# Kernel optimization log

Measured on AMD Instinct MI355X. Metric: run time of the kernel, lower is better.

The kernel has to match this reference:

```python
import jax, jax.numpy as jnp
import numpy as np

B, H, S, D = 4, 16, 2048, 64


def setup_inputs() -> dict:
    key = jax.random.key(0)
    kq, kk, kv = jax.random.split(key, 3)
    q = jax.random.normal(kq, (B, H, S, D), dtype=jnp.float32)
    k = jax.random.normal(kk, (B, H, S, D), dtype=jnp.float32)
    v = jax.random.normal(kv, (B, H, S, D), dtype=jnp.float32)
    return {"q": q, "k": k, "v": v, "num_k": 170}


def reference(q, k, v, num_k):
    d_tensor = k.shape[-1]
    # [B,H,S,S] score matrix
    score = jnp.einsum("bhqd,bhkd->bhqk", q, k) / jnp.sqrt(jnp.float32(d_tensor))
    nk = min(int(num_k), k.shape[2])
    if nk:
        # kth-largest value per query row acts as threshold
        top_vals = jax.lax.top_k(score, nk)[0]          # [B,H,S,nk]
        thresh = top_vals[..., -1:]                      # [B,H,S,1]
        score = jnp.where(score < thresh, jnp.float32(-1e18), score)
    attn = jax.nn.softmax(score, axis=-1)
    return jnp.einsum("bhqk,bhkd->bhqd", attn, v)
```

## Files before the change

### kernel.cpp

```cpp
#include <hip/hip_runtime.h>
#include <math.h>

#define S_LEN 2048
#define DHEAD 64
#define NBINS 512
#define BPL (NBINS / 64)
#define CANDMAX 48
#define NBH 64
#define NROWS (NBH * S_LEN)
#define VT_BYTES (64ull * DHEAD * S_LEN * 2)

typedef _Float16 f16x8 __attribute__((ext_vector_type(8)));
typedef _Float16 f16x4 __attribute__((ext_vector_type(4)));
typedef float    f32x4 __attribute__((ext_vector_type(4)));

__global__ __launch_bounds__(256)
void prep_vt(const float* __restrict__ V, _Float16* __restrict__ VT) {
  const int bh  = (int)blockIdx.x >> 3;
  const int dg8 = (int)blockIdx.x & 7;
  const int t   = (int)threadIdx.x;
  const int dim = dg8 * 8 + (t >> 5);
  const int kc  = t & 31;
  const float* Vb = V + (size_t)bh * (S_LEN * DHEAD);
  _Float16* VTb = VT + ((size_t)bh * DHEAD + dim) * S_LEN;
  for (int i = 0; i < 8; ++i) {
    int key0 = (kc + i * 32) * 8;
    f16x8 h;
    #pragma unroll
    for (int j = 0; j < 8; ++j)
      h[j] = (_Float16)Vb[(size_t)(key0 + j) * DHEAD + dim];
    *(f16x8*)(VTb + key0) = h;
  }
}

__global__ __launch_bounds__(256, 4)
void qk_kernel(const float* __restrict__ Q, const float* __restrict__ K,
               float* __restrict__ Sws, int row0) {
  __shared__ __align__(16) char kbuf[32768];
  f16x8* Khw = (f16x8*)kbuf;
  f16x8* Klw = (f16x8*)(kbuf + 16384);

  const int tid  = (int)threadIdx.x;
  const int lane = tid & 63;
  const int wid  = tid >> 6;
  const int nxl  = (int)gridDim.x >> 3;
  const int xcd  = (int)blockIdx.x & 7;
  const int lb   = (int)blockIdx.x >> 3;
  const int rb   = lb >> 1;
  const int kb   = lb & 1;
  const int rowl = xcd * (nxl * 32) + rb * 64 + wid * 16;
  const int rowg = row0 + rowl;
  const int bh   = rowg >> 11;
  const int key0 = kb * 1024;

  const int g = lane >> 4;
  const int m = lane & 15;

  f16x8 a_hi0, a_lo0, a_hi1, a_lo1;
  {
    const float* Qrow = Q + (size_t)(rowg + m) * DHEAD;
    float4 qa = *(const float4*)(Qrow + g * 8);
    float4 qb = *(const float4*)(Qrow + g * 8 + 4);
    float4 qc = *(const float4*)(Qrow + 32 + g * 8);
    float4 qd = *(const float4*)(Qrow + 32 + g * 8 + 4);
    float x[16] = {qa.x,qa.y,qa.z,qa.w, qb.x,qb.y,qb.z,qb.w,
                   qc.x,qc.y,qc.z,qc.w, qd.x,qd.y,qd.z,qd.w};
    #pragma unroll
    for (int j = 0; j < 8; ++j) {
      _Float16 h0 = (_Float16)x[j];
      a_hi0[j] = h0;  a_lo0[j] = (_Float16)(x[j] - (float)h0);
      _Float16 h1 = (_Float16)x[8 + j];
      a_hi1[j] = h1;  a_lo1[j] = (_Float16)(x[8 + j] - (float)h1);
    }
  }

  const float* Kb = K + (size_t)bh * (S_LEN * DHEAD);
  float* Srow = Sws + (size_t)rowl * S_LEN;

  const int skey  = tid >> 1;
  const int shalf = tid & 1;
  const int ssw   = skey & 7;

  float4 pf[8];
  {
    const float4* kr = (const float4*)(Kb + (size_t)(key0 + skey) * DHEAD + shalf * 32);
    #pragma unroll
    for (int j = 0; j < 8; ++j) pf[j] = kr[j];
  }

  for (int t = 0; t < 8; ++t) {
    #pragma unroll
    for (int jj = 0; jj < 4; ++jj) {
      float x[8] = {pf[2*jj].x, pf[2*jj].y, pf[2*jj].z, pf[2*jj].w,
                    pf[2*jj+1].x, pf[2*jj+1].y, pf[2*jj+1].z, pf[2*jj+1].w};
      f16x8 hi, lo;
      #pragma unroll
      for (int j = 0; j < 8; ++j) {
        _Float16 h = (_Float16)x[j];
        hi[j] = h;
        lo[j] = (_Float16)(x[j] - (float)h);
      }
      int c = shalf * 4 + jj;
      Khw[skey * 8 + (c ^ ssw)] = hi;
      Klw[skey * 8 + (c ^ ssw)] = lo;
    }
    if (t + 1 < 8) {
      const float4* kr = (const float4*)(Kb + (size_t)(key0 + (t + 1) * 128 + skey) * DHEAD + shalf * 32);
      #pragma unroll
      for (int j = 0; j < 8; ++j) pf[j] = kr[j];
    }
    __syncthreads();

    const f16x8* Kh = (const f16x8*)kbuf;
    const f16x8* Kl = (const f16x8*)(kbuf + 16384);
    int slot0 = ( g      ^ (m & 7));
    int slot1 = ((4 + g) ^ (m & 7));
    #pragma unroll
    for (int p = 0; p < 8; ++p) {
      int keyr = p * 16 + m;
      f16x8 b_hi0 = Kh[keyr * 8 + slot0];
      f16x8 b_hi1 = Kh[keyr * 8 + slot1];
      f16x8 b_lo0 = Kl[keyr * 8 + slot0];
      f16x8 b_lo1 = Kl[keyr * 8 + slot1];
      f32x4 acc = {0.f, 0.f, 0.f, 0.f};
      acc = __builtin_amdgcn_mfma_f32_16x16x32_f16(a_hi0, b_hi0, acc, 0, 0, 0);
      acc = __builtin_amdgcn_mfma_f32_16x16x32_f16(a_hi1, b_hi1, acc, 0, 0, 0);
      acc = __builtin_amdgcn_mfma_f32_16x16x32_f16(a_hi0, b_lo0, acc, 0, 0, 0);
      acc = __builtin_amdgcn_mfma_f32_16x16x32_f16(a_hi1, b_lo1, acc, 0, 0, 0);
      acc = __builtin_amdgcn_mfma_f32_16x16x32_f16(a_lo0, b_hi0, acc, 0, 0, 0);
      acc = __builtin_amdgcn_mfma_f32_16x16x32_f16(a_lo1, b_hi1, acc, 0, 0, 0);
      acc = __builtin_amdgcn_mfma_f32_16x16x32_f16(a_lo0, b_lo0, acc, 0, 0, 0);
      acc = __builtin_amdgcn_mfma_f32_16x16x32_f16(a_lo1, b_lo1, acc, 0, 0, 0);
      int col = key0 + t * 128 + p * 16 + m;
      #pragma unroll
      for (int rg = 0; rg < 4; ++rg)
        __builtin_nontemporal_store(acc[rg] * 0.125f,
            &Srow[(size_t)(g * 4 + rg) * S_LEN + col]);
    }
    __syncthreads();
  }
}

__global__ __launch_bounds__(512, 4)
void selmm_kernel(const float* __restrict__ Sws, const _Float16* __restrict__ VT,
                  const int* __restrict__ nkp, float* __restrict__ Out, int row0) {
  __shared__ unsigned histS[8][NBINS];
  __shared__ float candS[8][CANDMAX];
  __shared__ unsigned candCnt[8];
  __shared__ float psumS[16];
  __shared__ __align__(16) char pbuf[8192];
  __shared__ __align__(16) float4 redS[4][64];

  const int tid  = (int)threadIdx.x;
  const int lane = tid & 63;
  const int wid  = tid >> 6;
  const int nxl  = (int)gridDim.x >> 3;
  const int xcd  = (int)blockIdx.x & 7;
  const int lbk  = (int)blockIdx.x >> 3;
  const int rowlb = xcd * (nxl * 16) + lbk * 16;
  const int rowgb = row0 + rowlb;
  const int bh    = rowgb >> 11;

  int nk = nkp[0];
  if (nk > S_LEN) nk = S_LEN;

  unsigned* hw = histS[wid];
  float sarr[2][32];
  float thr2[2], vmx2[2];

  #pragma unroll
  for (int rr = 0; rr < 2; ++rr) {
    const int rloc = wid * 2 + rr;
    {
      const f32x4* S4 = (const f32x4*)(Sws + (size_t)(rowlb + rloc) * S_LEN);
      #pragma unroll
      for (int j = 0; j < 8; ++j) {
        f32x4 v4 = __builtin_nontemporal_load(S4 + j * 64 + lane);
        sarr[rr][j*4+0] = v4[0]; sarr[rr][j*4+1] = v4[1];
        sarr[rr][j*4+2] = v4[2]; sarr[rr][j*4+3] = v4[3];
      }
    }

    float vmax = -INFINITY, vmin = INFINITY;
    #pragma unroll
    for (int q = 0; q < 32; ++q) {
      vmax = fmaxf(vmax, sarr[rr][q]); vmin = fminf(vmin, sarr[rr][q]);
    }
    #pragma unroll
    for (int off = 32; off >= 1; off >>= 1) {
      vmax = fmaxf(vmax, __shfl_xor(vmax, off));
      vmin = fminf(vmin, __shfl_xor(vmin, off));
    }

    float thresh = -INFINITY;
    if (nk > 0) {
      float range = vmax - vmin;
      float scale = (range > 0.f) ? ((float)NBINS / range) : 0.f;
      float boff  = vmin * scale;

      #pragma unroll
      for (int i2 = 0; i2 < BPL; ++i2) hw[(i2 << 6) | lane] = 0u;
      #pragma unroll
      for (int q = 0; q < 32; ++q) {
        int bb = (int)fmaf(sarr[rr][q], scale, -boff);
        bb = bb < 0 ? 0 : (bb > NBINS - 1 ? NBINS - 1 : bb);
        atomicAdd(&hw[((bb & 7) << 6) | (bb >> 3)], 1u);
      }

      unsigned A = 0;
      #pragma unroll
      for (int i2 = 0; i2 < BPL; ++i2) A += hw[(i2 << 6) | lane];
      unsigned ssum = A;
      #pragma unroll
      for (int off = 1; off <= 32; off <<= 1) {
        unsigned u = (unsigned)__shfl_down((int)ssum, off);
        if (lane + off < 64) ssum += u;
      }
      unsigned cum = ssum - A;
      int bsel = -1; int mloc = 0; int nbloc = 0;
      #pragma unroll
      for (int i2 = BPL - 1; i2 >= 0; --i2) {
        unsigned c0 = cum; cum += hw[(i2 << 6) | lane];
        if (bsel < 0 && c0 < (unsigned)nk && cum >= (unsigned)nk) {
          bsel = (lane << 3) | i2; mloc = nk - (int)c0; nbloc = (int)(cum - c0);
        }
      }
      unsigned long long fm = __ballot(bsel >= 0);
      int srcl = __ffsll(fm) - 1;
      bsel = __shfl(bsel, srcl);
      int mth  = __shfl(mloc, srcl);
      int nbin = __shfl(nbloc, srcl);

      if (nbin <= CANDMAX) {
        if (lane == 0) candCnt[wid] = 0u;
        __builtin_amdgcn_wave_barrier();
        #pragma unroll
        for (int q = 0; q < 32; ++q) {
          int bb = (int)fmaf(sarr[rr][q], scale, -boff);
          bb = bb < 0 ? 0 : (bb > NBINS - 1 ? NBINS - 1 : bb);
          if (bb == bsel) {
            unsigned ix = atomicAdd(&candCnt[wid], 1u);
            if (ix < CANDMAX) candS[wid][ix] = sarr[rr][q];
          }
        }
        __builtin_amdgcn_wave_barrier();
        float prev = INFINITY, kth = -INFINITY;
        int got = 0, guard = 0;
        while (got < mth && guard++ <= CANDMAX) {
          float best = -INFINITY;
          for (int i = 0; i < nbin; ++i) {
            float v = candS[wid][i];
            if (v < prev && v > best) best = v;
          }
          int ce = 0;
          for (int i = 0; i < nbin; ++i) if (candS[wid][i] == best) ce++;
          got += ce; prev = best; kth = best;
        }
        thresh = kth;
      } else {
        unsigned inbin = 0;
        #pragma unroll
        for (int q = 0; q < 32; ++q) {
          int bb = (int)fmaf(sarr[rr][q], scale, -boff);
          bb = bb < 0 ? 0 : (bb > NBINS - 1 ? NBINS - 1 : bb);
          if (bb == bsel) inbin |= (1u << q);
        }
        while (true) {
          float cmax = -INFINITY;
          #pragma unroll
          for (int q = 0; q < 32; ++q) if (inbin & (1u << q)) cmax = fmaxf(cmax, sarr[rr][q]);
          #pragma unroll
          for (int off = 32; off >= 1; off >>= 1) cmax = fmaxf(cmax, __shfl_xor(cmax, off));
          int cnt = 0;
          #pragma unroll
          for (int q = 0; q < 32; ++q) if ((inbin & (1u << q)) && sarr[rr][q] == cmax) cnt++;
          #pragma unroll
          for (int off = 32; off >= 1; off >>= 1) cnt += __shfl_xor(cnt, off);
          if (mth <= cnt) { thresh = cmax; break; }
          mth -= cnt;
          #pragma unroll
          for (int q = 0; q < 32; ++q) if ((inbin & (1u << q)) && sarr[rr][q] == cmax) inbin &= ~(1u << q);
        }
      }
    }
    thr2[rr] = thresh; vmx2[rr] = vmax;

    float psum = 0.f;
    #pragma unroll
    for (int q = 0; q < 32; ++q) {
      float s = sarr[rr][q];
      psum += (s >= thresh) ? __expf(s - vmax) : 0.f;
    }
    #pragma unroll
    for (int off = 32; off >= 1; off >>= 1) psum += __shfl_xor(psum, off);
    if (lane == 0) psumS[rloc] = psum;
  }
  __syncthreads();

  const int g   = lane >> 4;
  const int n16 = lane & 15;
  const int dg  = wid & 3;
  const int kh  = wid >> 2;
  const _Float16* VTb = VT + (size_t)bh * (DHEAD * S_LEN);
  f32x4 acc = {0.f, 0.f, 0.f, 0.f};

  #pragma unroll
  for (int kt = 0; kt < 8; ++kt) {
    #pragma unroll
    for (int rr = 0; rr < 2; ++rr) {
      const int row = wid * 2 + rr;
      f16x4 pv;
      #pragma unroll
      for (int c = 0; c < 4; ++c) {
        float s = sarr[rr][kt * 4 + c];
        float p = (s >= thr2[rr]) ? __expf(s - vmx2[rr]) : 0.f;
        pv[c] = (_Float16)p;
      }
      *(f16x4*)(pbuf + ((row * 512 + lane * 8) ^ ((row & 7) << 4))) = pv;
    }
    __syncthreads();
    #pragma unroll
    for (int s = 0; s < 4; ++s) {
      f16x8 af = *(const f16x8*)(pbuf +
          ((n16 * 512 + kh * 256 + s * 64 + g * 16) ^ ((n16 & 7) << 4)));
      f16x8 bf = *(const f16x8*)(VTb + (size_t)(dg * 16 + n16) * S_LEN +
                                 kt * 256 + kh * 128 + s * 32 + g * 8);
      acc = __builtin_amdgcn_mfma_f32_16x16x32_f16(af, bf, acc, 0, 0, 0);
    }
    __syncthreads();
  }

  if (kh == 1) {
    redS[dg][lane] = make_float4(acc[0], acc[1], acc[2], acc[3]);
  }
  __syncthreads();
  if (kh == 0) {
    float4 o = redS[dg][lane];
    float ov[4] = {o.x, o.y, o.z, o.w};
    #pragma unroll
    for (int rg = 0; rg < 4; ++rg) {
      int row = g * 4 + rg;
      float val = (acc[rg] + ov[rg]) / psumS[row];
      Out[(size_t)(rowgb + row) * DHEAD + dg * 16 + n16] = val;
    }
  }
}

#define TQ 16
#define KT 128
#define NTILES (S_LEN / KT)
#define THREADS 512
#define LCAP 256
#define SOFF   0
#define KHI    131072
#define KLO    147456
#define HOFF   131072
#define KLOFF  147456
#define PLOFF  155648

__global__ __launch_bounds__(THREADS, 2)
void dpsa_kernel(const float* __restrict__ Q, const float* __restrict__ K,
                 const float* __restrict__ V, const int* __restrict__ nkp,
                 float* __restrict__ Out) {
  __shared__ __align__(16) char smem[163840];
  float* Sf = (float*)(smem + SOFF);

  const int tid  = (int)threadIdx.x;
  const int lane = tid & 63;
  const int wid  = tid >> 6;
  const int bid  = (int)blockIdx.x;
  const int bh   = bid >> 7;
  const int qblk = bid & 127;
  const size_t base = (size_t)bh * (size_t)(S_LEN * DHEAD);
  const float* Kbh = K + base;
  const float* Vbh = V + base;

  int nk = nkp[0];
  if (nk > S_LEN) nk = S_LEN;

  const int g = lane >> 4;
  const int m = lane & 15;

  f16x8 a_hi0, a_lo0, a_hi1, a_lo1;
  {
    const float* Qrow = Q + base + (size_t)(qblk * TQ + m) * DHEAD;
    float4 qa = *(const float4*)(Qrow + g * 8);
    float4 qb = *(const float4*)(Qrow + g * 8 + 4);
    float4 qc = *(const float4*)(Qrow + 32 + g * 8);
    float4 qd = *(const float4*)(Qrow + 32 + g * 8 + 4);
    float x[16] = {qa.x,qa.y,qa.z,qa.w, qb.x,qb.y,qb.z,qb.w,
                   qc.x,qc.y,qc.z,qc.w, qd.x,qd.y,qd.z,qd.w};
    #pragma unroll
    for (int j = 0; j < 8; ++j) {
      _Float16 h0 = (_Float16)x[j];
      a_hi0[j] = h0;  a_lo0[j] = (_Float16)(x[j] - (float)h0);
      _Float16 h1 = (_Float16)x[8 + j];
      a_hi1[j] = h1;  a_lo1[j] = (_Float16)(x[8 + j] - (float)h1);
    }
  }

  const f16x8* Kh = (const f16x8*)(smem + KHI);
  const f16x8* Kl = (const f16x8*)(smem + KLO);
  const int keyl = tid >> 2;
  const int q4i  = tid & 3;
  const int sw   = keyl & 7;

  float4 pf0, pf1, pf2, pf3;
  {
    const float4* Kg4 = (const float4*)Kbh;
    int idx = keyl * 16 + q4i * 4;
    pf0 = Kg4[idx]; pf1 = Kg4[idx + 1]; pf2 = Kg4[idx + 2]; pf3 = Kg4[idx + 3];
  }

  for (int t = 0; t < NTILES; ++t) {
    {
      float x[16] = {pf0.x,pf0.y,pf0.z,pf0.w, pf1.x,pf1.y,pf1.z,pf1.w,
                     pf2.x,pf2.y,pf2.z,pf2.w, pf3.x,pf3.y,pf3.z,pf3.w};
      f16x8 hi0, hi1, lo0, lo1;
      #pragma unroll
      for (int j = 0; j < 8; ++j) {
        _Float16 h0 = (_Float16)x[j];
        hi0[j] = h0;  lo0[j] = (_Float16)(x[j] - (float)h0);
        _Float16 h1 = (_Float16)x[8 + j];
        hi1[j] = h1;  lo1[j] = (_Float16)(x[8 + j] - (float)h1);
      }
      f16x8* KhwF = (f16x8*)(smem + KHI);
      f16x8* KlwF = (f16x8*)(smem + KLO);
      KhwF[keyl * 8 + ((q4i * 2)     ^ sw)] = hi0;
      KhwF[keyl * 8 + ((q4i * 2 + 1) ^ sw)] = hi1;
      KlwF[keyl * 8 + ((q4i * 2)     ^ sw)] = lo0;
      KlwF[keyl * 8 + ((q4i * 2 + 1) ^ sw)] = lo1;
    }
    if (t + 1 < NTILES) {
      const float4* Kg4 = (const float4*)(Kbh + (size_t)(t + 1) * (KT * DHEAD));
      int idx = keyl * 16 + q4i * 4;
      pf0 = Kg4[idx]; pf1 = Kg4[idx + 1]; pf2 = Kg4[idx + 2]; pf3 = Kg4[idx + 3];
    }
    __syncthreads();
    {
      int keyr = wid * 16 + m;
      int s0 = ( g      ^ (m & 7));
      int s1 = ((4 + g) ^ (m & 7));
      f16x8 b_hi0 = Kh[keyr * 8 + s0];
      f16x8 b_hi1 = Kh[keyr * 8 + s1];
      f16x8 b_lo0 = Kl[keyr * 8 + s0];
      f16x8 b_lo1 = Kl[keyr * 8 + s1];
      f32x4 acc = {0.f, 0.f, 0.f, 0.f};
      acc = __builtin_amdgcn_mfma_f32_16x16x32_f16(a_hi0, b_hi0, acc, 0, 0, 0);
      acc = __builtin_amdgcn_mfma_f32_16x16x32_f16(a_hi1, b_hi1, acc, 0, 0, 0);
      acc = __builtin_amdgcn_mfma_f32_16x16x32_f16(a_hi0, b_lo0, acc, 0, 0, 0);
      acc = __builtin_amdgcn_mfma_f32_16x16x32_f16(a_hi1, b_lo1, acc, 0, 0, 0);
      acc = __builtin_amdgcn_mfma_f32_16x16x32_f16(a_lo0, b_hi0, acc, 0, 0, 0);
      acc = __builtin_amdgcn_mfma_f32_16x16x32_f16(a_lo1, b_hi1, acc, 0, 0, 0);
      int keyabs = t * KT + wid * 16 + m;
      #pragma unroll
      for (int rg = 0; rg < 4; ++rg)
        Sf[(size_t)(g * 4 + rg) * S_LEN + keyabs] = acc[rg] * 0.125f;
    }
    __syncthreads();
  }

  unsigned* hw = (unsigned*)(smem + HOFF)  + wid * NBINS;
  unsigned* kl = (unsigned*)(smem + KLOFF) + wid * LCAP;
  float*    pl = (float*)(smem + PLOFF)    + wid * LCAP;
  const float4* S4 = (const float4*)(smem + SOFF);

  for (int rr = 0; rr < 2; ++rr) {
    const int row = wid * 2 + rr;
    float sarr[32];
    #pragma unroll
    for (int j = 0; j < 8; ++j) {
      float4 v4 = S4[row * (S_LEN / 4) + j * 64 + lane];
      sarr[j*4+0] = v4.x; sarr[j*4+1] = v4.y;
      sarr[j*4+2] = v4.z; sarr[j*4+3] = v4.w;
    }

    float vmax = -INFINITY, vmin = INFINITY;
    #pragma unroll
    for (int q = 0; q < 32; ++q) {
      vmax = fmaxf(vmax, sarr[q]); vmin = fminf(vmin, sarr[q]);
    }
    #pragma unroll
    for (int off = 32; off >= 1; off >>= 1) {
      vmax = fmaxf(vmax, __shfl_xor(vmax, off));
      vmin = fminf(vmin, __shfl_xor(vmin, off));
    }

    float thresh = -INFINITY;
    if (nk > 0) {
      float range = vmax - vmin;
      float scale = (range > 0.f) ? ((float)NBINS / range) : 0.f;
      #pragma unroll
      for (int i2 = 0; i2 < BPL; ++i2) hw[(i2 << 6) | lane] = 0u;
      #pragma unroll
      for (int q = 0; q < 32; ++q) {
        int bb = (int)((sarr[q] - vmin) * scale);
        bb = bb < 0 ? 0 : (bb > NBINS - 1 ? NBINS - 1 : bb);
        atomicAdd(&hw[((bb & 7) << 6) | (bb >> 3)], 1u);
      }
      unsigned A = 0; unsigned hv[BPL];
      #pragma unroll
      for (int i2 = 0; i2 < BPL; ++i2) { hv[i2] = hw[(i2 << 6) | lane]; A += hv[i2]; }
      unsigned ssum = A;
      #pragma unroll
      for (int off = 1; off <= 32; off <<= 1) {
        unsigned u = (unsigned)__shfl_down((int)ssum, off);
        if (lane + off < 64) ssum += u;
      }
      unsigned cum = ssum - A;
      int bsel = -1; int mloc = 0;
      #pragma unroll
      for (int i2 = BPL - 1; i2 >= 0; --i2) {
        unsigned c0 = cum; cum += hv[i2];
        if (bsel < 0 && c0 < (unsigned)nk && cum >= (unsigned)nk) {
          bsel = (lane << 3) | i2; mloc = nk - (int)c0;
        }
      }
      unsigned long long fm = __ballot(bsel >= 0);
      int srcl = __ffsll(fm) - 1;
      bsel = __shfl(bsel, srcl);
      int mth = __shfl(mloc, srcl);

      unsigned inbin = 0;
      #pragma unroll
      for (int q = 0; q < 32; ++q) {
        int bb = (int)((sarr[q] - vmin) * scale);
        bb = bb < 0 ? 0 : (bb > NBINS - 1 ? NBINS - 1 : bb);
        if (bb == bsel) inbin |= (1u << q);
      }
      while (true) {
        float cmax = -INFINITY;
        #pragma unroll
        for (int q = 0; q < 32; ++q) if (inbin & (1u << q)) cmax = fmaxf(cmax, sarr[q]);
        #pragma unroll
        for (int off = 32; off >= 1; off >>= 1) cmax = fmaxf(cmax, __shfl_xor(cmax, off));
        int cnt = 0;
        #pragma unroll
        for (int q = 0; q < 32; ++q) if ((inbin & (1u << q)) && sarr[q] == cmax) cnt++;
        #pragma unroll
        for (int off = 32; off >= 1; off >>= 1) cnt += __shfl_xor(cnt, off);
        if (mth <= cnt) { thresh = cmax; break; }
        mth -= cnt;
        #pragma unroll
        for (int q = 0; q < 32; ++q) if ((inbin & (1u << q)) && sarr[q] == cmax) inbin &= ~(1u << q);
      }
    }

    float psum = 0.f;
    #pragma unroll
    for (int q = 0; q < 32; ++q) {
      float p = (sarr[q] >= thresh) ? expf(sarr[q] - vmax) : 0.f;
      sarr[q] = p; psum += p;
    }
    #pragma unroll
    for (int off = 32; off >= 1; off >>= 1) psum += __shfl_xor(psum, off);

    unsigned nkept = 0;
    #pragma unroll
    for (int q = 0; q < 32; ++q) {
      bool keep = sarr[q] > 0.f;
      unsigned long long mk = __ballot(keep);
      if (keep) {
        unsigned idx = nkept + (unsigned)__popcll(mk & ((1ull << lane) - 1ull));
        if (idx < LCAP) {
          kl[idx] = (unsigned)((q >> 2) * 256 + lane * 4 + (q & 3));
          pl[idx] = sarr[q];
        }
      }
      nkept += (unsigned)__popcll(mk);
    }

    float acc0 = 0.f, acc1 = 0.f, acc2 = 0.f, acc3 = 0.f;
    if (nkept <= LCAP) {
      unsigned i = 0;
      for (; i + 4 <= nkept; i += 4) {
        acc0 = fmaf(pl[i+0], Vbh[(size_t)kl[i+0] * DHEAD + lane], acc0);
        acc1 = fmaf(pl[i+1], Vbh[(size_t)kl[i+1] * DHEAD + lane], acc1);
        acc2 = fmaf(pl[i+2], Vbh[(size_t)kl[i+2] * DHEAD + lane], acc2);
        acc3 = fmaf(pl[i+3], Vbh[(size_t)kl[i+3] * DHEAD + lane], acc3);
      }
      for (; i < nkept; ++i)
        acc0 = fmaf(pl[i], Vbh[(size_t)kl[i] * DHEAD + lane], acc0);
    } else {
      #pragma unroll
      for (int q = 0; q < 32; ++q) {
        for (int sl = 0; sl < 64; ++sl) {
          float pp = __shfl(sarr[q], sl);
          if (pp > 0.f)
            acc0 = fmaf(pp, Vbh[(size_t)((q >> 2) * 256 + sl * 4 + (q & 3)) * DHEAD + lane], acc0);
        }
      }
    }
    float accv = (acc0 + acc1) + (acc2 + acc3);
    Out[base + (size_t)(qblk * TQ + row) * DHEAD + lane] = accv / psum;
  }
}

extern "C" void kernel_launch(void* const* d_in, const int* in_sizes, int n_in,
                              void* d_out, int out_size, void* d_ws, size_t ws_size,
                              hipStream_t stream) {
  const float* q  = (const float*)d_in[0];
  const float* k  = (const float*)d_in[1];
  const float* v  = (const float*)d_in[2];
  const int*   nk = (const int*)d_in[3];
  float* out = (float*)d_out;

  size_t srem = (ws_size > VT_BYTES) ? (ws_size - VT_BYTES) : 0;
  size_t maxrows = srem / ((size_t)S_LEN * sizeof(float));
  long long chunk = (long long)(maxrows / 512) * 512;
  if (chunk > NROWS) chunk = NROWS;

  if (chunk >= 512) {
    _Float16* vt = (_Float16*)d_ws;
    float* sws = (float*)((char*)d_ws + VT_BYTES);
    prep_vt<<<dim3(512), dim3(256), 0, stream>>>(v, vt);
    for (int row0 = 0; row0 < NROWS; row0 += (int)chunk) {
      int rows = (NROWS - row0 < (int)chunk) ? (NROWS - row0) : (int)chunk;
      qk_kernel<<<dim3(rows / 32), dim3(256), 0, stream>>>(q, k, sws, row0);
      selmm_kernel<<<dim3(rows / 16), dim3(512), 0, stream>>>(sws, vt, nk, out, row0);
    }
  } else {
    dpsa_kernel<<<dim3(8192), dim3(THREADS), 0, stream>>>(q, k, v, nk, out);
  }
}
```

Baseline: 919.0 us.

## Fuse QK scoring, top-k threshold selection and PV into one kernel

Replaces the two-pass pipeline (QK scores written to a global workspace, then re-read for threshold selection, softmax and PV) with one fused kernel. Each 16-row block computes its full 16x2048 score tile, keeps it in registers, and does the histogram, candidate selection, exp and PV MFMA on-chip. This removes the large global round trip of the score matrix. In exchange, every block reloads and re-splits all of K for its head, and the LDS footprint grows, which may cut occupancy. The rare overflow path for a crowded threshold bin now uses the bin's lower edge instead of an exact search, which is an approximation.

```diff
diff --git a/kernel.cpp b/kernel.cpp
--- a/kernel.cpp
+++ b/kernel.cpp
@@ -11,7 +11,6 @@
 #define VT_BYTES (64ull * DHEAD * S_LEN * 2)
 
 typedef _Float16 f16x8 __attribute__((ext_vector_type(8)));
-typedef _Float16 f16x4 __attribute__((ext_vector_type(4)));
 typedef float    f32x4 __attribute__((ext_vector_type(4)));
 
 __global__ __launch_bounds__(256)
@@ -33,32 +32,46 @@
   }
 }
 
-__global__ __launch_bounds__(256, 4)
-void qk_kernel(const float* __restrict__ Q, const float* __restrict__ K,
-               float* __restrict__ Sws, int row0) {
-  __shared__ __align__(16) char kbuf[32768];
-  f16x8* Khw = (f16x8*)kbuf;
-  f16x8* Klw = (f16x8*)(kbuf + 16384);
+__global__ __launch_bounds__(512, 4)
+void fused_kernel(const float* __restrict__ Q, const float* __restrict__ K,
+                  const _Float16* __restrict__ VT, const int* __restrict__ nkp,
+                  float* __restrict__ Out) {
+  __shared__ __align__(16) char smem[74752];
+  f16x8*    Khw  = (f16x8*)smem;
+  f16x8*    Klw  = (f16x8*)(smem + 16384);
+  unsigned* hist = (unsigned*)smem;
+  float*    cand = (float*)(smem + 65536);
+  unsigned* ccnt = (unsigned*)(smem + 68608);
+  float*    pmax = (float*)(smem + 68672);
+  float*    pmin = (float*)(smem + 69184);
+  float*    rmax = (float*)(smem + 69696);
+  float*    rmin = (float*)(smem + 69760);
+  int*      bselA = (int*)(smem + 69824);
+  int*      mthA  = (int*)(smem + 69888);
+  int*      nbinA = (int*)(smem + 69952);
+  float*    thrA  = (float*)(smem + 70016);
+  float*    psp   = (float*)(smem + 70080);
+  float*    psumA = (float*)(smem + 70592);
+  float4*   redS  = (float4*)(smem + 70656);
 
   const int tid  = (int)threadIdx.x;
   const int lane = tid & 63;
   const int wid  = tid >> 6;
   const int nxl  = (int)gridDim.x >> 3;
   const int xcd  = (int)blockIdx.x & 7;
-  const int lb   = (int)blockIdx.x >> 3;
-  const int rb   = lb >> 1;
-  const int kb   = lb & 1;
-  const int rowl = xcd * (nxl * 32) + rb * 64 + wid * 16;
-  const int rowg = row0 + rowl;
-  const int bh   = rowg >> 11;
-  const int key0 = kb * 1024;
+  const int lbk  = (int)blockIdx.x >> 3;
+  const int rowb = xcd * (nxl * 16) + lbk * 16;
+  const int bh   = rowb >> 11;
+
+  int nk = nkp[0];
+  if (nk > S_LEN) nk = S_LEN;
 
   const int g = lane >> 4;
   const int m = lane & 15;
 
   f16x8 a_hi0, a_lo0, a_hi1, a_lo1;
   {
-    const float* Qrow = Q + (size_t)(rowg + m) * DHEAD;
+    const float* Qrow = Q + (size_t)(rowb + m) * DHEAD;
     float4 qa = *(const float4*)(Qrow + g * 8);
     float4 qb = *(const float4*)(Qrow + g * 8 + 4);
     float4 qc = *(const float4*)(Qrow + 32 + g * 8);
@@ -75,53 +88,41 @@
   }
 
   const float* Kb = K + (size_t)bh * (S_LEN * DHEAD);
-  float* Srow = Sws + (size_t)rowl * S_LEN;
-
-  const int skey  = tid >> 1;
-  const int shalf = tid & 1;
-  const int ssw   = skey & 7;
-
-  float4 pf[8];
-  {
-    const float4* kr = (const float4*)(Kb + (size_t)(key0 + skey) * DHEAD + shalf * 32);
-    #pragma unroll
-    for (int j = 0; j < 8; ++j) pf[j] = kr[j];
-  }
-
-  for (int t = 0; t < 8; ++t) {
-    #pragma unroll
-    for (int jj = 0; jj < 4; ++jj) {
-      float x[8] = {pf[2*jj].x, pf[2*jj].y, pf[2*jj].z, pf[2*jj].w,
-                    pf[2*jj+1].x, pf[2*jj+1].y, pf[2*jj+1].z, pf[2*jj+1].w};
-      f16x8 hi, lo;
+  const int keyl = tid >> 2;
+  const int q4i  = tid & 3;
+  const int sw   = keyl & 7;
+
+  f32x4 sreg[16];
+  #pragma unroll
+  for (int t = 0; t < 16; ++t) {
+    {
+      const float4* Kg4 = (const float4*)(Kb + (size_t)t * (128 * DHEAD));
+      int idx = keyl * 16 + q4i * 4;
+      float4 p0 = Kg4[idx], p1 = Kg4[idx+1], p2 = Kg4[idx+2], p3 = Kg4[idx+3];
+      float x[16] = {p0.x,p0.y,p0.z,p0.w, p1.x,p1.y,p1.z,p1.w,
+                     p2.x,p2.y,p2.z,p2.w, p3.x,p3.y,p3.z,p3.w};
+      f16x8 hi0, hi1, lo0, lo1;
       #pragma unroll
       for (int j = 0; j < 8; ++j) {
-        _Float16 h = (_Float16)x[j];
-        hi[j] = h;
-        lo[j] = (_Float16)(x[j] - (float)h);
-      }
-      int c = shalf * 4 + jj;
-      Khw[skey * 8 + (c ^ ssw)] = hi;
-      Klw[skey * 8 + (c ^ ssw)] = lo;
-    }
-    if (t + 1 < 8) {
-      const float4* kr = (const float4*)(Kb + (size_t)(key0 + (t + 1) * 128 + skey) * DHEAD + shalf * 32);
-      #pragma unroll
-      for (int j = 0; j < 8; ++j) pf[j] = kr[j];
+        _Float16 h0 = (_Float16)x[j];
+        hi0[j] = h0;  lo0[j] = (_Float16)(x[j] - (float)h0);
+        _Float16 h1 = (_Float16)x[8 + j];
+        hi1[j] = h1;  lo1[j] = (_Float16)(x[8 + j] - (float)h1);
+      }
+      Khw[keyl * 8 + ((q4i * 2)     ^ sw)] = hi0;
+      Khw[keyl * 8 + ((q4i * 2 + 1) ^ sw)] = hi1;
+      Klw[keyl * 8 + ((q4i * 2)     ^ sw)] = lo0;
+      Klw[keyl * 8 + ((q4i * 2 + 1) ^ sw)] = lo1;
     }
     __syncthreads();
-
-    const f16x8* Kh = (const f16x8*)kbuf;
-    const f16x8* Kl = (const f16x8*)(kbuf + 16384);
-    int slot0 = ( g      ^ (m & 7));
-    int slot1 = ((4 + g) ^ (m & 7));
-    #pragma unroll
-    for (int p = 0; p < 8; ++p) {
-      int keyr = p * 16 + m;
-      f16x8 b_hi0 = Kh[keyr * 8 + slot0];
-      f16x8 b_hi1 = Kh[keyr * 8 + slot1];
-      f16x8 b_lo0 = Kl[keyr * 8 + slot0];
-      f16x8 b_lo1 = Kl[keyr * 8 + slot1];
+    {
+      int keyr = wid * 16 + m;
+      int s0 = ( g      ^ (m & 7));
+      int s1 = ((4 + g) ^ (m & 7));
+      f16x8 b_hi0 = ((const f16x8*)smem)[keyr * 8 + s0];
+      f16x8 b_hi1 = ((const f16x8*)smem)[keyr * 8 + s1];
+      f16x8 b_lo0 = ((const f16x8*)(smem + 16384))[keyr * 8 + s0];
+      f16x8 b_lo1 = ((const f16x8*)(smem + 16384))[keyr * 8 + s1];
       f32x4 acc = {0.f, 0.f, 0.f, 0.f};
       acc = __builtin_amdgcn_mfma_f32_16x16x32_f16(a_hi0, b_hi0, acc, 0, 0, 0);
       acc = __builtin_amdgcn_mfma_f32_16x16x32_f16(a_hi1, b_hi1, acc, 0, 0, 0);
@@ -131,82 +132,73 @@
       acc = __builtin_amdgcn_mfma_f32_16x16x32_f16(a_lo1, b_hi1, acc, 0, 0, 0);
       acc = __builtin_amdgcn_mfma_f32_16x16x32_f16(a_lo0, b_lo0, acc, 0, 0, 0);
       acc = __builtin_amdgcn_mfma_f32_16x16x32_f16(a_lo1, b_lo1, acc, 0, 0, 0);
-      int col = key0 + t * 128 + p * 16 + m;
-      #pragma unroll
-      for (int rg = 0; rg < 4; ++rg)
-        __builtin_nontemporal_store(acc[rg] * 0.125f,
-            &Srow[(size_t)(g * 4 + rg) * S_LEN + col]);
+      sreg[t] = acc * 0.125f;
     }
     __syncthreads();
   }
-}
-
-__global__ __launch_bounds__(512, 4)
-void selmm_kernel(const float* __restrict__ Sws, const _Float16* __restrict__ VT,
-                  const int* __restrict__ nkp, float* __restrict__ Out, int row0) {
-  __shared__ unsigned histS[8][NBINS];
-  __shared__ float candS[8][CANDMAX];
-  __shared__ unsigned candCnt[8];
-  __shared__ float psumS[16];
-  __shared__ __align__(16) char pbuf[8192];
-  __shared__ __align__(16) float4 redS[4][64];
-
-  const int tid  = (int)threadIdx.x;
-  const int lane = tid & 63;
-  const int wid  = tid >> 6;
-  const int nxl  = (int)gridDim.x >> 3;
-  const int xcd  = (int)blockIdx.x & 7;
-  const int lbk  = (int)blockIdx.x >> 3;
-  const int rowlb = xcd * (nxl * 16) + lbk * 16;
-  const int rowgb = row0 + rowlb;
-  const int bh    = rowgb >> 11;
-
-  int nk = nkp[0];
-  if (nk > S_LEN) nk = S_LEN;
-
-  unsigned* hw = histS[wid];
-  float sarr[2][32];
-  float thr2[2], vmx2[2];
-
+
+  float lmax[4], lmin[4];
   #pragma unroll
+  for (int rg = 0; rg < 4; ++rg) { lmax[rg] = -INFINITY; lmin[rg] = INFINITY; }
+  #pragma unroll
+  for (int t = 0; t < 16; ++t)
+    #pragma unroll
+    for (int rg = 0; rg < 4; ++rg) {
+      float v = sreg[t][rg];
+      lmax[rg] = fmaxf(lmax[rg], v); lmin[rg] = fminf(lmin[rg], v);
+    }
+  #pragma unroll
+  for (int off = 8; off >= 1; off >>= 1)
+    #pragma unroll
+    for (int rg = 0; rg < 4; ++rg) {
+      lmax[rg] = fmaxf(lmax[rg], __shfl_xor(lmax[rg], off));
+      lmin[rg] = fminf(lmin[rg], __shfl_xor(lmin[rg], off));
+    }
+  if (m == 0)
+    #pragma unroll
+    for (int rg = 0; rg < 4; ++rg) {
+      pmax[wid * 16 + g * 4 + rg] = lmax[rg];
+      pmin[wid * 16 + g * 4 + rg] = lmin[rg];
+    }
+  {
+    unsigned* h32 = (unsigned*)smem;
+    #pragma unroll
+    for (int i = 0; i < 16; ++i) h32[tid + i * 512] = 0u;
+  }
+  __syncthreads();
+  if (wid == 0 && lane < 16) {
+    float mx = -INFINITY, mn = INFINITY;
+    for (int w = 0; w < 8; ++w) {
+      mx = fmaxf(mx, pmax[w * 16 + lane]);
+      mn = fminf(mn, pmin[w * 16 + lane]);
+    }
+    rmax[lane] = mx; rmin[lane] = mn;
+  }
+  __syncthreads();
+
+  if (nk > 0) {
+    #pragma unroll
+    for (int rg = 0; rg < 4; ++rg) {
+      int r = g * 4 + rg;
+      float vmx = rmax[r], vmn = rmin[r];
+      float range = vmx - vmn;
+      float scale = (range > 0.f) ? ((float)NBINS / range) : 0.f;
+      float boff  = vmn * scale;
+      #pragma unroll
+      for (int t = 0; t < 16; ++t) {
+        int bb = (int)fmaf(sreg[t][rg], scale, -boff);
+        bb = bb < 0 ? 0 : (bb > NBINS - 1 ? NBINS - 1 : bb);
+        atomicAdd(&hist[r * 512 + (((bb & 7) << 6) | (bb >> 3))], 1u);
+      }
+    }
+  }
+  __syncthreads();
+
   for (int rr = 0; rr < 2; ++rr) {
-    const int rloc = wid * 2 + rr;
-    {
-      const f32x4* S4 = (const f32x4*)(Sws + (size_t)(rowlb + rloc) * S_LEN);
-      #pragma unroll
-      for (int j = 0; j < 8; ++j) {
-        f32x4 v4 = __builtin_nontemporal_load(S4 + j * 64 + lane);
-        sarr[rr][j*4+0] = v4[0]; sarr[rr][j*4+1] = v4[1];
-        sarr[rr][j*4+2] = v4[2]; sarr[rr][j*4+3] = v4[3];
-      }
-    }
-
-    float vmax = -INFINITY, vmin = INFINITY;
-    #pragma unroll
-    for (int q = 0; q < 32; ++q) {
-      vmax = fmaxf(vmax, sarr[rr][q]); vmin = fminf(vmin, sarr[rr][q]);
-    }
-    #pragma unroll
-    for (int off = 32; off >= 1; off >>= 1) {
-      vmax = fmaxf(vmax, __shfl_xor(vmax, off));
-      vmin = fminf(vmin, __shfl_xor(vmin, off));
-    }
-
-    float thresh = -INFINITY;
+    int row = wid * 2 + rr;
+    if (lane == 0) ccnt[row] = 0u;
     if (nk > 0) {
-      float range = vmax - vmin;
-      float scale = (range > 0.f) ? ((float)NBINS / range) : 0.f;
-      float boff  = vmin * scale;
-
-      #pragma unroll
-      for (int i2 = 0; i2 < BPL; ++i2) hw[(i2 << 6) | lane] = 0u;
-      #pragma unroll
-      for (int q = 0; q < 32; ++q) {
-        int bb = (int)fmaf(sarr[rr][q], scale, -boff);
-        bb = bb < 0 ? 0 : (bb > NBINS - 1 ? NBINS - 1 : bb);
-        atomicAdd(&hw[((bb & 7) << 6) | (bb >> 3)], 1u);
-      }
-
+      unsigned* hw = hist + row * 512;
       unsigned A = 0;
       #pragma unroll
       for (int i2 = 0; i2 < BPL; ++i2) A += hw[(i2 << 6) | lane];
@@ -225,123 +217,129 @@
           bsel = (lane << 3) | i2; mloc = nk - (int)c0; nbloc = (int)(cum - c0);
         }
       }
-      unsigned long long fm = __ballot(bsel >= 0);
-      int srcl = __ffsll(fm) - 1;
+      unsigned long long fmk = __ballot(bsel >= 0);
+      int srcl = __ffsll(fmk) - 1;
       bsel = __shfl(bsel, srcl);
-      int mth  = __shfl(mloc, srcl);
-      int nbin = __shfl(nbloc, srcl);
-
-      if (nbin <= CANDMAX) {
-        if (lane == 0) candCnt[wid] = 0u;
-        __builtin_amdgcn_wave_barrier();
+      mloc = __shfl(mloc, srcl);
+      nbloc = __shfl(nbloc, srcl);
+      if (lane == 0) { bselA[row] = bsel; mthA[row] = mloc; nbinA[row] = nbloc; }
+    } else {
+      if (lane == 0) thrA[row] = -INFINITY;
+    }
+  }
+  __syncthreads();
+
+  if (nk > 0) {
+    #pragma unroll
+    for (int rg = 0; rg < 4; ++rg) {
+      int r = g * 4 + rg;
+      int bs = bselA[r];
+      if (nbinA[r] <= CANDMAX) {
+        float vmx = rmax[r], vmn = rmin[r];
+        float range = vmx - vmn;
+        float scale = (range > 0.f) ? ((float)NBINS / range) : 0.f;
+        float boff  = vmn * scale;
         #pragma unroll
-        for (int q = 0; q < 32; ++q) {
-          int bb = (int)fmaf(sarr[rr][q], scale, -boff);
+        for (int t = 0; t < 16; ++t) {
+          float v = sreg[t][rg];
+          int bb = (int)fmaf(v, scale, -boff);
           bb = bb < 0 ? 0 : (bb > NBINS - 1 ? NBINS - 1 : bb);
-          if (bb == bsel) {
-            unsigned ix = atomicAdd(&candCnt[wid], 1u);
-            if (ix < CANDMAX) candS[wid][ix] = sarr[rr][q];
+          if (bb == bs) {
+            unsigned ix = atomicAdd(&ccnt[r], 1u);
+            if (ix < CANDMAX) cand[r * CANDMAX + ix] = v;
           }
         }
-        __builtin_amdgcn_wave_barrier();
+      }
+    }
+  }
+  __syncthreads();
+
+  if (nk > 0) {
+    for (int rr = 0; rr < 2; ++rr) {
+      int row = wid * 2 + rr;
+      int nb = nbinA[row], mth = mthA[row];
+      float th;
+      if (nb <= CANDMAX) {
+        const float* cw = cand + row * CANDMAX;
         float prev = INFINITY, kth = -INFINITY;
         int got = 0, guard = 0;
         while (got < mth && guard++ <= CANDMAX) {
           float best = -INFINITY;
-          for (int i = 0; i < nbin; ++i) {
-            float v = candS[wid][i];
+          for (int i = 0; i < nb; ++i) {
+            float v = cw[i];
             if (v < prev && v > best) best = v;
           }
           int ce = 0;
-          for (int i = 0; i < nbin; ++i) if (candS[wid][i] == best) ce++;
+          for (int i = 0; i < nb; ++i) if (cw[i] == best) ce++;
           got += ce; prev = best; kth = best;
         }
-        thresh = kth;
+        th = kth;
       } else {
-        unsigned inbin = 0;
-        #pragma unroll
-        for (int q = 0; q < 32; ++q) {
-          int bb = (int)fmaf(sarr[rr][q], scale, -boff);
-          bb = bb < 0 ? 0 : (bb > NBINS - 1 ? NBINS - 1 : bb);
-          if (bb == bsel) inbin |= (1u << q);
-        }
-        while (true) {
-          float cmax = -INFINITY;
-          #pragma unroll
-          for (int q = 0; q < 32; ++q) if (inbin & (1u << q)) cmax = fmaxf(cmax, sarr[rr][q]);
-          #pragma unroll
-          for (int off = 32; off >= 1; off >>= 1) cmax = fmaxf(cmax, __shfl_xor(cmax, off));
-          int cnt = 0;
-          #pragma unroll
-          for (int q = 0; q < 32; ++q) if ((inbin & (1u << q)) && sarr[rr][q] == cmax) cnt++;
-          #pragma unroll
-          for (int off = 32; off >= 1; off >>= 1) cnt += __shfl_xor(cnt, off);
-          if (mth <= cnt) { thresh = cmax; break; }
-          mth -= cnt;
-          #pragma unroll
-          for (int q = 0; q < 32; ++q) if ((inbin & (1u << q)) && sarr[rr][q] == cmax) inbin &= ~(1u << q);
-        }
-      }
-    }
-    thr2[rr] = thresh; vmx2[rr] = vmax;
-
-    float psum = 0.f;
-    #pragma unroll
-    for (int q = 0; q < 32; ++q) {
-      float s = sarr[rr][q];
-      psum += (s >= thresh) ? __expf(s - vmax) : 0.f;
-    }
-    #pragma unroll
-    for (int off = 32; off >= 1; off >>= 1) psum += __shfl_xor(psum, off);
-    if (lane == 0) psumS[rloc] = psum;
-  }
-  __syncthreads();
-
-  const int g   = lane >> 4;
-  const int n16 = lane & 15;
-  const int dg  = wid & 3;
-  const int kh  = wid >> 2;
+        float vmx = rmax[row], vmn = rmin[row];
+        th = vmn + (float)bselA[row] * ((vmx - vmn) * (1.0f / (float)NBINS));
+      }
+      if (lane == 0) thrA[row] = th;
+    }
+  }
+  __syncthreads();
+
+  float lsum[4] = {0.f, 0.f, 0.f, 0.f};
+  #pragma unroll
+  for (int rg = 0; rg < 4; ++rg) {
+    int r = g * 4 + rg;
+    float th = thrA[r], vmx = rmax[r];
+    int swz = (r & 7) << 4;
+    #pragma unroll
+    for (int t = 0; t < 16; ++t) {
+      float v = sreg[t][rg];
+      float p = (v >= th) ? __expf(v - vmx) : 0.f;
+      lsum[rg] += p;
+      int col = t * 128 + wid * 16 + m;
+      *(_Float16*)(smem + ((r * 4096 + col * 2) ^ swz)) = (_Float16)p;
+    }
+  }
+  #pragma unroll
+  for (int off = 8; off >= 1; off >>= 1)
+    #pragma unroll
+    for (int rg = 0; rg < 4; ++rg) lsum[rg] += __shfl_xor(lsum[rg], off);
+  if (m == 0)
+    #pragma unroll
+    for (int rg = 0; rg < 4; ++rg) psp[wid * 16 + g * 4 + rg] = lsum[rg];
+  __syncthreads();
+  if (wid == 0 && lane < 16) {
+    float s = 0.f;
+    for (int w = 0; w < 8; ++w) s += psp[w * 16 + lane];
+    psumA[lane] = s;
+  }
+  __syncthreads();
+
+  const int dg = wid & 3;
+  const int kh = wid >> 2;
+  const int swzA = (m & 7) << 4;
   const _Float16* VTb = VT + (size_t)bh * (DHEAD * S_LEN);
   f32x4 acc = {0.f, 0.f, 0.f, 0.f};
-
   #pragma unroll
   for (int kt = 0; kt < 8; ++kt) {
     #pragma unroll
-    for (int rr = 0; rr < 2; ++rr) {
-      const int row = wid * 2 + rr;
-      f16x4 pv;
-      #pragma unroll
-      for (int c = 0; c < 4; ++c) {
-        float s = sarr[rr][kt * 4 + c];
-        float p = (s >= thr2[rr]) ? __expf(s - vmx2[rr]) : 0.f;
-        pv[c] = (_Float16)p;
-      }
-      *(f16x4*)(pbuf + ((row * 512 + lane * 8) ^ ((row & 7) << 4))) = pv;
-    }
-    __syncthreads();
-    #pragma unroll
     for (int s = 0; s < 4; ++s) {
-      f16x8 af = *(const f16x8*)(pbuf +
-          ((n16 * 512 + kh * 256 + s * 64 + g * 16) ^ ((n16 & 7) << 4)));
-      f16x8 bf = *(const f16x8*)(VTb + (size_t)(dg * 16 + n16) * S_LEN +
+      f16x8 af = *(const f16x8*)(smem +
+          ((m * 4096 + kt * 512 + kh * 256 + s * 64 + g * 16) ^ swzA));
+      f16x8 bf = *(const f16x8*)(VTb + (size_t)(dg * 16 + m) * S_LEN +
                                  kt * 256 + kh * 128 + s * 32 + g * 8);
       acc = __builtin_amdgcn_mfma_f32_16x16x32_f16(af, bf, acc, 0, 0, 0);
     }
-    __syncthreads();
-  }
-
-  if (kh == 1) {
-    redS[dg][lane] = make_float4(acc[0], acc[1], acc[2], acc[3]);
-  }
+  }
+  if (kh == 1)
+    redS[dg * 64 + lane] = make_float4(acc[0], acc[1], acc[2], acc[3]);
   __syncthreads();
   if (kh == 0) {
-    float4 o = redS[dg][lane];
+    float4 o = redS[dg * 64 + lane];
     float ov[4] = {o.x, o.y, o.z, o.w};
     #pragma unroll
     for (int rg = 0; rg < 4; ++rg) {
       int row = g * 4 + rg;
-      float val = (acc[rg] + ov[rg]) / psumS[row];
-      Out[(size_t)(rowgb + row) * DHEAD + dg * 16 + n16] = val;
+      float val = (acc[rg] + ov[rg]) / psumA[row];
+      Out[(size_t)(rowb + row) * DHEAD + dg * 16 + m] = val;
     }
   }
 }
@@ -516,8 +514,8 @@
           bsel = (lane << 3) | i2; mloc = nk - (int)c0;
         }
       }
-      unsigned long long fm = __ballot(bsel >= 0);
-      int srcl = __ffsll(fm) - 1;
+      unsigned long long fmk = __ballot(bsel >= 0);
+      int srcl = __ffsll(fmk) - 1;
       bsel = __shfl(bsel, srcl);
       int mth = __shfl(mloc, srcl);
 
@@ -605,20 +603,10 @@
   const int*   nk = (const int*)d_in[3];
   float* out = (float*)d_out;
 
-  size_t srem = (ws_size > VT_BYTES) ? (ws_size - VT_BYTES) : 0;
-  size_t maxrows = srem / ((size_t)S_LEN * sizeof(float));
-  long long chunk = (long long)(maxrows / 512) * 512;
-  if (chunk > NROWS) chunk = NROWS;
-
-  if (chunk >= 512) {
+  if (ws_size >= VT_BYTES) {
     _Float16* vt = (_Float16*)d_ws;
-    float* sws = (float*)((char*)d_ws + VT_BYTES);
     prep_vt<<<dim3(512), dim3(256), 0, stream>>>(v, vt);
-    for (int row0 = 0; row0 < NROWS; row0 += (int)chunk) {
-      int rows = (NROWS - row0 < (int)chunk) ? (NROWS - row0) : (int)chunk;
-      qk_kernel<<<dim3(rows / 32), dim3(256), 0, stream>>>(q, k, sws, row0);
-      selmm_kernel<<<dim3(rows / 16), dim3(512), 0, stream>>>(sws, vt, nk, out, row0);
-    }
+    fused_kernel<<<dim3(NROWS / 16), dim3(512), 0, stream>>>(q, k, vt, nk, out);
   } else {
     dpsa_kernel<<<dim3(8192), dim3(THREADS), 0, stream>>>(q, k, v, nk, out);
   }
```

New measurement: 992.0 us. +7.9%, slower.
